# Kernel optimization log

Measured on AMD Instinct MI355X. Metric: run time of the kernel, lower is better.

The kernel has to match this reference:

```python
import jax, jax.numpy as jnp
import numpy as np

V, D, H, KV, L, FF, HD = 32000, 768, 12, 4, 4, 2048, 64
N_REP = H // KV  # 3
EPS = 1e-6
ROPE_THETA = 10000.0


def setup_inputs() -> dict:
    key = jax.random.key(0)
    ks = jax.random.split(key, 12)
    s = 0.02
    return {
        'idx': jax.random.randint(ks[0], (1, 2048), 0, V),
        'embed': jax.random.normal(ks[1], (V, D), jnp.float32) * s,
        'ln1_w': jnp.ones((L, D), jnp.float32),
        'Wq': jax.random.normal(ks[2], (L, D, H * HD), jnp.float32) * s,
        'Wk': jax.random.normal(ks[3], (L, D, KV * HD), jnp.float32) * s,
        'Wv': jax.random.normal(ks[4], (L, D, KV * HD), jnp.float32) * s,
        'Wo': jax.random.normal(ks[5], (L, H * HD, D), jnp.float32) * s,
        'ln2_w': jnp.ones((L, D), jnp.float32),
        'Wg': jax.random.normal(ks[6], (L, D, FF), jnp.float32) * s,
        'Wu': jax.random.normal(ks[7], (L, D, FF), jnp.float32) * s,
        'Wd': jax.random.normal(ks[8], (L, FF, D), jnp.float32) * s,
        'normf_w': jnp.ones((D,), jnp.float32),
    }


def _rms(x, w):
    xf = x.astype(jnp.float32)
    var = jnp.mean(xf * xf, axis=-1, keepdims=True)
    return w * (xf * jax.lax.rsqrt(var + EPS)).astype(x.dtype)


def _rotate_half(x):
    x1, x2 = x[..., : x.shape[-1] // 2], x[..., x.shape[-1] // 2:]
    return jnp.concatenate((-x2, x1), axis=-1)


def reference(idx, embed, ln1_w, Wq, Wk, Wv, Wo, ln2_w, Wg, Wu, Wd, normf_w):
    B, T = idx.shape
    x = embed[idx]  # [B,T,D]

    # RoPE tables: cos/sin [1,1,T,HD]
    inv_freq = 1.0 / (ROPE_THETA ** (jnp.arange(0, HD, 2, dtype=jnp.float32) / HD))
    pos = jnp.arange(T, dtype=jnp.float32)
    freqs = pos[:, None] * inv_freq[None, :]          # [T,HD/2]
    emb = jnp.concatenate((freqs, freqs), axis=-1)     # [T,HD]
    cos = jnp.cos(emb)[None, None].astype(x.dtype)
    sin = jnp.sin(emb)[None, None].astype(x.dtype)

    causal = jnp.tril(jnp.ones((T, T), bool))[None, None]  # [1,1,T,T]
    scale = 1.0 / np.sqrt(HD)

    for l in range(L):
        # --- attention ---
        h = _rms(x, ln1_w[l])
        q = (h @ Wq[l]).reshape(B, T, H, HD).transpose(0, 2, 1, 3)   # [B,H,T,HD]
        k = (h @ Wk[l]).reshape(B, T, KV, HD).transpose(0, 2, 1, 3)  # [B,KV,T,HD]
        v = (h @ Wv[l]).reshape(B, T, KV, HD).transpose(0, 2, 1, 3)
        q = q * cos + _rotate_half(q) * sin
        k = k * cos + _rotate_half(k) * sin
        k = jnp.repeat(k, N_REP, axis=1)  # [B,H,T,HD]
        v = jnp.repeat(v, N_REP, axis=1)
        scores = jnp.einsum('bhqd,bhkd->bhqk', q, k) * scale
        scores = jnp.where(causal, scores, -jnp.inf)
        probs = jax.nn.softmax(scores.astype(jnp.float32), axis=-1).astype(q.dtype)
        attn = jnp.einsum('bhqk,bhkd->bhqd', probs, v)
        attn = attn.transpose(0, 2, 1, 3).reshape(B, T, H * HD)
        x = x + attn @ Wo[l]
        # --- gated MLP ---
        h = _rms(x, ln2_w[l])
        x = x + (jax.nn.gelu(h @ Wg[l], approximate=True) * (h @ Wu[l])) @ Wd[l]

    x = _rms(x, normf_w)
    logits = (x @ embed.T).astype(jnp.float32)  # tied lm_head
    return logits
```

## Files before the change

### kernel.cpp

```cpp
#include <hip/hip_runtime.h>

#define TSEQ 2048
#define DM   768
#define NH   12
#define NKV  4
#define HD   64
#define FFD  2048
#define NL   4
#define VOC  32000
#define QKVN 1280

typedef __attribute__((ext_vector_type(8))) short short8;
typedef __attribute__((ext_vector_type(4))) float f32x4;

__device__ __forceinline__ unsigned short f2b(float f) {
  unsigned int u = __float_as_uint(f);
  u += 0x7fffu + ((u >> 16) & 1u);
  return (unsigned short)(u >> 16);
}
__device__ __forceinline__ float b2f(unsigned short u) {
  return __uint_as_float(((unsigned int)u) << 16);
}
__device__ __forceinline__ unsigned int packbf(float a, float b) {
  return (unsigned int)f2b(a) | ((unsigned int)f2b(b) << 16);
}

__device__ __forceinline__ void gl16(const unsigned short* g, unsigned short* l) {
  __builtin_amdgcn_global_load_lds(
      (const __attribute__((address_space(1))) void*)g,
      (__attribute__((address_space(3))) void*)l, 16, 0, 0);
}

__global__ void cast_bf16_kernel(const float* __restrict__ src,
                                 unsigned short* __restrict__ dst, int n4) {
  int i = blockIdx.x * blockDim.x + threadIdx.x;
  if (i >= n4) return;
  float4 v = ((const float4*)src)[i];
  uint2 o; o.x = packbf(v.x, v.y); o.y = packbf(v.z, v.w);
  ((uint2*)dst)[i] = o;
}

__global__ void rope_tab_kernel(float2* __restrict__ tab) {
  int i = blockIdx.x * blockDim.x + threadIdx.x;
  int pos = i >> 5, d = i & 31;
  float inv = exp2f(-(float)d * (13.287712379549449f / 32.0f));
  float sv, cv; sincosf((float)pos * inv, &sv, &cv);
  tab[i] = make_float2(cv, sv);
}

__global__ void transpose_all_kernel(const float* __restrict__ Wq, const float* __restrict__ Wk,
                                     const float* __restrict__ Wv, const float* __restrict__ Wo,
                                     const float* __restrict__ Wg, const float* __restrict__ Wu,
                                     const float* __restrict__ Wd, unsigned short* __restrict__ wts,
                                     size_t LW) {
  __shared__ float tile[32][33];
  int r = blockIdx.x, l = blockIdx.z;
  const float* src; size_t sstr, doff; int K, N, nx;
  if (r < 576)       { src = Wq; sstr = 589824;  doff = 0;                          K = 768;  N = 768;  nx = 24; }
  else if (r < 768)  { src = Wk; sstr = 196608;  doff = 768ull * 768;               K = 768;  N = 256;  nx = 8;  r -= 576; }
  else if (r < 960)  { src = Wv; sstr = 196608;  doff = 1024ull * 768;              K = 768;  N = 256;  nx = 8;  r -= 768; }
  else if (r < 1536) { src = Wo; sstr = 589824;  doff = (size_t)QKVN * DM;          K = 768;  N = 768;  nx = 24; r -= 960; }
  else if (r < 3072) { src = Wg; sstr = 1572864; doff = (size_t)QKVN * DM + (size_t)DM * DM;
                       K = 768;  N = 2048; nx = 64; r -= 1536; }
  else if (r < 4608) { src = Wu; sstr = 1572864; doff = (size_t)QKVN * DM + (size_t)DM * DM + (size_t)FFD * DM;
                       K = 768;  N = 2048; nx = 64; r -= 3072; }
  else               { src = Wd; sstr = 1572864; doff = (size_t)QKVN * DM + (size_t)DM * DM + 2ull * FFD * DM;
                       K = 2048; N = 768;  nx = 24; r -= 4608; }
  int bx = r % nx, by = r / nx;
  src += (size_t)l * sstr;
  unsigned short* dst = wts + (size_t)l * LW + doff;
  int n0 = bx * 32, k0 = by * 32;
  int tx = threadIdx.x, ty = threadIdx.y;
  #pragma unroll
  for (int i = 0; i < 4; ++i) {
    int rr = ty + i * 8;
    tile[rr][tx] = src[(size_t)(k0 + rr) * N + n0 + tx];
  }
  __syncthreads();
  #pragma unroll
  for (int i = 0; i < 4; ++i) {
    int rr = ty + i * 8;
    dst[(size_t)(n0 + rr) * K + k0 + tx] = f2b(tile[tx][rr]);
  }
}

__global__ void gather_kernel(const int* __restrict__ idx,
                              const float* __restrict__ embed,
                              float* __restrict__ x) {
  int row = blockIdx.x; int t = threadIdx.x;
  int id = idx[row];
  ((float4*)(x + (size_t)row * DM))[t] = ((const float4*)(embed + (size_t)id * DM))[t];
}

__global__ void rmsnorm_kernel(const float* __restrict__ x,
                               const float* __restrict__ w,
                               unsigned short* __restrict__ out) {
  int row = blockIdx.x; int t = threadIdx.x;
  const float* xr = x + (size_t)row * DM;
  float v0 = xr[t], v1 = xr[t + 256], v2 = xr[t + 512];
  float s = v0*v0 + v1*v1 + v2*v2;
  #pragma unroll
  for (int off = 1; off < 64; off <<= 1) s += __shfl_xor(s, off);
  __shared__ float red[4];
  if ((t & 63) == 0) red[t >> 6] = s;
  __syncthreads();
  float tot = red[0] + red[1] + red[2] + red[3];
  float rs = rsqrtf(tot * (1.0f / DM) + 1e-6f);
  unsigned short* orow = out + (size_t)row * DM;
  orow[t]       = f2b(w[t]       * v0 * rs);
  orow[t + 256] = f2b(w[t + 256] * v1 * rs);
  orow[t + 512] = f2b(w[t + 512] * v2 * rs);
}

__global__ __launch_bounds__(512, 1) void gemm_l8_kernel(
    const unsigned short* __restrict__ A, const unsigned short* __restrict__ Bt,
    float* __restrict__ C, int N, int K) {
  __shared__ unsigned short lds[2][2][256 * 64];
  const int NT = K >> 6;
  int bid = blockIdx.x, nwg = gridDim.x;
  int wgid = (bid & 7) * (nwg >> 3) + (bid >> 3);
  int m0 = (wgid & 7) * 256;
  int n0 = (wgid >> 3) * 256;
  int tid = threadIdx.x;
  int lane = tid & 63, w = tid >> 6;
  int wm = w >> 2, wn = w & 3;
  int al = lane & 15, ag = lane >> 4;
  int swz = (al & 7) << 3;

  int rA = tid >> 3;
  int cK = ((tid & 7) * 8) ^ ((rA & 7) << 3);
  const unsigned short* Ag = A + (size_t)(m0 + rA) * K + cK;
  const unsigned short* Bg = Bt + (size_t)(n0 + rA) * K + cK;

  f32x4 acc[8][4];
  #pragma unroll
  for (int i = 0; i < 8; ++i)
    #pragma unroll
    for (int n = 0; n < 4; ++n) acc[i][n] = (f32x4){0.f, 0.f, 0.f, 0.f};

  #define STAGE(kt, c) { \
    size_t ko = (size_t)(kt) * 64; \
    unsigned short* dA = &lds[(c)][0][0] + w * 512; \
    unsigned short* dB = &lds[(c)][1][0] + w * 512; \
    gl16(Ag + (size_t)0   * K + ko, dA);            \
    gl16(Ag + (size_t)64  * K + ko, dA + 4096);     \
    gl16(Ag + (size_t)128 * K + ko, dA + 8192);     \
    gl16(Ag + (size_t)192 * K + ko, dA + 12288);    \
    gl16(Bg + (size_t)0   * K + ko, dB);            \
    gl16(Bg + (size_t)64  * K + ko, dB + 4096);     \
    gl16(Bg + (size_t)128 * K + ko, dB + 8192);     \
    gl16(Bg + (size_t)192 * K + ko, dB + 12288);    \
  }

  STAGE(0, 0);
  STAGE(1, 1);
  asm volatile("s_waitcnt vmcnt(8)" ::: "memory");
  __builtin_amdgcn_s_barrier();

  for (int t = 0; t < NT; ++t) {
    int cur = t & 1;
    const unsigned short* La = &lds[cur][0][0];
    const unsigned short* Lb = &lds[cur][1][0];
    short8 a0[8], b0[4], a1[8], b1[4];
    #pragma unroll
    for (int i = 0; i < 4; ++i)
      a0[i] = *(const short8*)&La[(wm*128 + i*16 + al)*64 + ((ag*8) ^ swz)];
    #pragma unroll
    for (int n = 0; n < 4; ++n)
      b0[n] = *(const short8*)&Lb[(wn*64 + n*16 + al)*64 + ((ag*8) ^ swz)];
    #pragma unroll
    for (int i = 4; i < 8; ++i)
      a0[i] = *(const short8*)&La[(wm*128 + i*16 + al)*64 + ((ag*8) ^ swz)];
    asm volatile("s_waitcnt lgkmcnt(4)" ::: "memory");
    __builtin_amdgcn_sched_barrier(0);
    #pragma unroll
    for (int i = 0; i < 4; ++i)
      #pragma unroll
      for (int n = 0; n < 4; ++n)
        acc[i][n] = __builtin_amdgcn_mfma_f32_16x16x32_bf16(a0[i], b0[n], acc[i][n], 0, 0, 0);
    #pragma unroll
    for (int n = 0; n < 4; ++n)
      b1[n] = *(const short8*)&Lb[(wn*64 + n*16 + al)*64 + ((32 + ag*8) ^ swz)];
    #pragma unroll
    for (int i = 0; i < 4; ++i)
      a1[i] = *(const short8*)&La[(wm*128 + i*16 + al)*64 + ((32 + ag*8) ^ swz)];
    asm volatile("s_waitcnt lgkmcnt(8)" ::: "memory");
    __builtin_amdgcn_sched_barrier(0);
    #pragma unroll
    for (int i = 4; i < 8; ++i)
      #pragma unroll
      for (int n = 0; n < 4; ++n)
        acc[i][n] = __builtin_amdgcn_mfma_f32_16x16x32_bf16(a0[i], b0[n], acc[i][n], 0, 0, 0);
    #pragma unroll
    for (int i = 4; i < 8; ++i)
      a1[i] = *(const short8*)&La[(wm*128 + i*16 + al)*64 + ((32 + ag*8) ^ swz)];
    asm volatile("s_waitcnt lgkmcnt(4)" ::: "memory");
    __builtin_amdgcn_sched_barrier(0);
    #pragma unroll
    for (int i = 0; i < 4; ++i)
      #pragma unroll
      for (int n = 0; n < 4; ++n)
        acc[i][n] = __builtin_amdgcn_mfma_f32_16x16x32_bf16(a1[i], b1[n], acc[i][n], 0, 0, 0);
    asm volatile("s_waitcnt lgkmcnt(0)" ::: "memory");
    __builtin_amdgcn_sched_barrier(0);
    __builtin_amdgcn_s_barrier();
    if (t + 2 < NT) STAGE(t + 2, cur);
    __builtin_amdgcn_s_setprio(1);
    #pragma unroll
    for (int i = 4; i < 8; ++i)
      #pragma unroll
      for (int n = 0; n < 4; ++n)
        acc[i][n] = __builtin_amdgcn_mfma_f32_16x16x32_bf16(a1[i], b1[n], acc[i][n], 0, 0, 0);
    __builtin_amdgcn_s_setprio(0);
    if (t + 2 < NT) { asm volatile("s_waitcnt vmcnt(8)" ::: "memory"); }
    else            { asm volatile("s_waitcnt vmcnt(0)" ::: "memory"); }
    __builtin_amdgcn_s_barrier();
  }
  #undef STAGE

  #pragma unroll
  for (int i = 0; i < 8; ++i)
    #pragma unroll
    for (int r = 0; r < 4; ++r) {
      float* Cr = C + (size_t)(m0 + wm*128 + i*16 + ag*4 + r) * N + n0 + wn*64 + al;
      #pragma unroll
      for (int n = 0; n < 4; ++n) Cr[n * 16] = acc[i][n][r];
    }
}

__global__ __launch_bounds__(512) void gemm_p8_kernel(
    const unsigned short* __restrict__ A, const unsigned short* __restrict__ Bt,
    float* __restrict__ C, int N, int K, int Kc) {
  __shared__ unsigned short lds[2][2][128 * 64];
  const int NT = Kc >> 6;
  int bid = blockIdx.x, nwg = gridDim.x;
  int wgid = (bid & 7) * (nwg >> 3) + (bid >> 3);
  int m0 = (wgid & 15) * 128;
  int n0 = (wgid >> 4) * 128;
  int tid = threadIdx.x;
  int lane = tid & 63, w = tid >> 6;
  int wm = w >> 2, wn = w & 3;
  int al = lane & 15, ag = lane >> 4;
  int swz = (al & 7) << 3;

  size_t koff = (size_t)blockIdx.y * Kc;
  int rp = 8 * w + (lane >> 3);
  int cK = ((lane & 7) * 8) ^ ((lane >> 3) << 3);
  const unsigned short* Ag = A + (size_t)(m0 + rp) * K + koff + cK;
  const unsigned short* Bg = Bt + (size_t)(n0 + rp) * K + koff + cK;

  f32x4 acc[4][2];
  #pragma unroll
  for (int i = 0; i < 4; ++i)
    #pragma unroll
    for (int n = 0; n < 2; ++n) acc[i][n] = (f32x4){0.f, 0.f, 0.f, 0.f};

  #define STAGE(kt, c) { \
    size_t ko = (size_t)(kt) * 64; \
    unsigned short* dA = &lds[(c)][0][0] + w * 512; \
    unsigned short* dB = &lds[(c)][1][0] + w * 512; \
    gl16(Ag + ko,                 dA);        \
    gl16(Ag + (size_t)64*K + ko,  dA + 4096); \
    gl16(Bg + ko,                 dB);        \
    gl16(Bg + (size_t)64*K + ko,  dB + 4096); \
  }

  STAGE(0, 0);
  STAGE(1, 1);
  asm volatile("s_waitcnt vmcnt(4)" ::: "memory");
  __builtin_amdgcn_s_barrier();

  for (int t = 0; t < NT; ++t) {
    int cur = t & 1;
    const unsigned short* La = &lds[cur][0][0];
    const unsigned short* Lb = &lds[cur][1][0];
    short8 a0[4], b0[2], a1[4], b1[2];
    #pragma unroll
    for (int i = 0; i < 4; ++i)
      a0[i] = *(const short8*)&La[(wm*64 + i*16 + al)*64 + ((ag*8) ^ swz)];
    #pragma unroll
    for (int n = 0; n < 2; ++n)
      b0[n] = *(const short8*)&Lb[(wn*32 + n*16 + al)*64 + ((ag*8) ^ swz)];
    #pragma unroll
    for (int i = 0; i < 4; ++i)
      a1[i] = *(const short8*)&La[(wm*64 + i*16 + al)*64 + ((32 + ag*8) ^ swz)];
    #pragma unroll
    for (int n = 0; n < 2; ++n)
      b1[n] = *(const short8*)&Lb[(wn*32 + n*16 + al)*64 + ((32 + ag*8) ^ swz)];
    asm volatile("s_waitcnt lgkmcnt(6)" ::: "memory");
    __builtin_amdgcn_sched_barrier(0);
    #pragma unroll
    for (int i = 0; i < 4; ++i)
      #pragma unroll
      for (int n = 0; n < 2; ++n)
        acc[i][n] = __builtin_amdgcn_mfma_f32_16x16x32_bf16(a0[i], b0[n], acc[i][n], 0, 0, 0);
    asm volatile("s_waitcnt lgkmcnt(0)" ::: "memory");
    __builtin_amdgcn_sched_barrier(0);
    __builtin_amdgcn_s_barrier();
    if (t + 2 < NT) STAGE(t + 2, cur);
    __builtin_amdgcn_s_setprio(1);
    #pragma unroll
    for (int i = 0; i < 4; ++i)
      #pragma unroll
      for (int n = 0; n < 2; ++n)
        acc[i][n] = __builtin_amdgcn_mfma_f32_16x16x32_bf16(a1[i], b1[n], acc[i][n], 0, 0, 0);
    __builtin_amdgcn_s_setprio(0);
    if (t + 2 < NT) { asm volatile("s_waitcnt vmcnt(4)" ::: "memory"); }
    else            { asm volatile("s_waitcnt vmcnt(0)" ::: "memory"); }
    __builtin_amdgcn_s_barrier();
  }
  #undef STAGE

  #pragma unroll
  for (int i = 0; i < 4; ++i)
    #pragma unroll
    for (int r = 0; r < 4; ++r) {
      float* Cr = C + (size_t)(m0 + wm*64 + i*16 + ag*4 + r) * N + n0 + wn*32 + al;
      #pragma unroll
      for (int n = 0; n < 2; ++n) atomicAdd(&Cr[n * 16], acc[i][n][r]);
    }
}

__device__ __forceinline__ float gelu_t(float x) {
  float x3 = x * x * x;
  return 0.5f * x * (1.0f + tanhf(0.7978845608028654f * (x + 0.044715f * x3)));
}

__global__ __launch_bounds__(512) void gemm_gu8_kernel(
    const unsigned short* __restrict__ A, const unsigned short* __restrict__ BtG,
    const unsigned short* __restrict__ BtU, unsigned short* __restrict__ Cm) {
  __shared__ unsigned short lds[2][3][128 * 64];
  const int K = DM;
  const int NT = K >> 6;
  int bid = blockIdx.x, nwg = gridDim.x;
  int wgid = (bid & 7) * (nwg >> 3) + (bid >> 3);
  int m0 = (wgid & 15) * 128;
  int n0 = (wgid >> 4) * 128;
  int tid = threadIdx.x;
  int lane = tid & 63, w = tid >> 6;
  int wm = w >> 2, wn = w & 3;
  int al = lane & 15, ag = lane >> 4;
  int swz = (al & 7) << 3;

  int rp = 8 * w + (lane >> 3);
  int cK = ((lane & 7) * 8) ^ ((lane >> 3) << 3);
  const unsigned short* Ag = A + (size_t)(m0 + rp) * K + cK;
  const unsigned short* Gg = BtG + (size_t)(n0 + rp) * K + cK;
  const unsigned short* Ug = BtU + (size_t)(n0 + rp) * K + cK;

  f32x4 accg[4][2], accu[4][2];
  #pragma unroll
  for (int i = 0; i < 4; ++i)
    #pragma unroll
    for (int n = 0; n < 2; ++n) {
      accg[i][n] = (f32x4){0.f, 0.f, 0.f, 0.f};
      accu[i][n] = (f32x4){0.f, 0.f, 0.f, 0.f};
    }

  #define STAGE(kt, c) { \
    size_t ko = (size_t)(kt) * 64; \
    unsigned short* dA = &lds[(c)][0][0] + w * 512; \
    unsigned short* dG = &lds[(c)][1][0] + w * 512; \
    unsigned short* dU = &lds[(c)][2][0] + w * 512; \
    gl16(Ag + ko,                 dA);        \
    gl16(Ag + (size_t)64*K + ko,  dA + 4096); \
    gl16(Gg + ko,                 dG);        \
    gl16(Gg + (size_t)64*K + ko,  dG + 4096); \
    gl16(Ug + ko,                 dU);        \
    gl16(Ug + (size_t)64*K + ko,  dU + 4096); \
  }

  STAGE(0, 0);
  STAGE(1, 1);
  asm volatile("s_waitcnt vmcnt(6)" ::: "memory");
  __builtin_amdgcn_s_barrier();

  for (int t = 0; t < NT; ++t) {
    int cur = t & 1;
    const unsigned short* La = &lds[cur][0][0];
    const unsigned short* Lg = &lds[cur][1][0];
    const unsigned short* Lu = &lds[cur][2][0];
    short8 a0[4], g0[2], u0[2], a1[4], g1[2], u1[2];
    #pragma unroll
    for (int i = 0; i < 4; ++i)
      a0[i] = *(const short8*)&La[(wm*64 + i*16 + al)*64 + ((ag*8) ^ swz)];
    #pragma unroll
    for (int n = 0; n < 2; ++n) {
      g0[n] = *(const short8*)&Lg[(wn*32 + n*16 + al)*64 + ((ag*8) ^ swz)];
      u0[n] = *(const short8*)&Lu[(wn*32 + n*16 + al)*64 + ((ag*8) ^ swz)];
    }
    #pragma unroll
    for (int i = 0; i < 4; ++i)
      a1[i] = *(const short8*)&La[(wm*64 + i*16 + al)*64 + ((32 + ag*8) ^ swz)];
    #pragma unroll
    for (int n = 0; n < 2; ++n) {
      g1[n] = *(const short8*)&Lg[(wn*32 + n*16 + al)*64 + ((32 + ag*8) ^ swz)];
      u1[n] = *(const short8*)&Lu[(wn*32 + n*16 + al)*64 + ((32 + ag*8) ^ swz)];
    }
    asm volatile("s_waitcnt lgkmcnt(8)" ::: "memory");
    __builtin_amdgcn_sched_barrier(0);
    #pragma unroll
    for (int i = 0; i < 4; ++i)
      #pragma unroll
      for (int n = 0; n < 2; ++n) {
        accg[i][n] = __builtin_amdgcn_mfma_f32_16x16x32_bf16(a0[i], g0[n], accg[i][n], 0, 0, 0);
        accu[i][n] = __builtin_amdgcn_mfma_f32_16x16x32_bf16(a0[i], u0[n], accu[i][n], 0, 0, 0);
      }
    asm volatile("s_waitcnt lgkmcnt(0)" ::: "memory");
    __builtin_amdgcn_sched_barrier(0);
    __builtin_amdgcn_s_barrier();
    if (t + 2 < NT) STAGE(t + 2, cur);
    __builtin_amdgcn_s_setprio(1);
    #pragma unroll
    for (int i = 0; i < 4; ++i)
      #pragma unroll
      for (int n = 0; n < 2; ++n) {
        accg[i][n] = __builtin_amdgcn_mfma_f32_16x16x32_bf16(a1[i], g1[n], accg[i][n], 0, 0, 0);
        accu[i][n] = __builtin_amdgcn_mfma_f32_16x16x32_bf16(a1[i], u1[n], accu[i][n], 0, 0, 0);
      }
    __builtin_amdgcn_s_setprio(0);
    if (t + 2 < NT) { asm volatile("s_waitcnt vmcnt(6)" ::: "memory"); }
    else            { asm volatile("s_waitcnt vmcnt(0)" ::: "memory"); }
    __builtin_amdgcn_s_barrier();
  }
  #undef STAGE

  #pragma unroll
  for (int i = 0; i < 4; ++i)
    #pragma unroll
    for (int r = 0; r < 4; ++r) {
      unsigned short* Cr = Cm + (size_t)(m0 + wm*64 + i*16 + ag*4 + r) * FFD + n0 + wn*32 + al;
      #pragma unroll
      for (int n = 0; n < 2; ++n)
        Cr[n * 16] = f2b(gelu_t(accg[i][n][r]) * accu[i][n][r]);
    }
}

__global__ __launch_bounds__(256) void gemm_qkv_kernel(
    const unsigned short* __restrict__ A, const unsigned short* __restrict__ Bt,
    unsigned short* __restrict__ C, unsigned short* __restrict__ vT,
    const float2* __restrict__ rope_tab) {
  const int N = QKVN, K = DM;
  __shared__ unsigned short As[128 * 40];
  __shared__ unsigned short Bs[128 * 40];
  int bid = blockIdx.x, nwg = gridDim.x;
  int wgid = (bid & 7) * (nwg >> 3) + (bid >> 3);
  int m0 = (wgid & 15) * 128;
  int n0 = (wgid >> 4) * 128;
  int tid = threadIdx.x;
  int lane = tid & 63, wave = tid >> 6;
  int wr = (wave >> 1) * 64, wc = (wave & 1) * 64;
  int l16 = lane & 15, lk8 = (lane >> 4) * 8;
  f32x4 acc[4][4];
  #pragma unroll
  for (int m = 0; m < 4; ++m)
    #pragma unroll
    for (int n = 0; n < 4; ++n) acc[m][n] = (f32x4){0.f, 0.f, 0.f, 0.f};
  const unsigned short* Abase = A + (size_t)m0 * K;
  const unsigned short* Bbase = Bt + (size_t)n0 * K;
  int r0 = tid >> 2;
  int c0 = (tid & 3) * 8;
  for (int k0 = 0; k0 < K; k0 += 32) {
    uint4 a0 = *(const uint4*)(Abase + (size_t)r0 * K + k0 + c0);
    uint4 a1 = *(const uint4*)(Abase + (size_t)(r0 + 64) * K + k0 + c0);
    uint4 b0 = *(const uint4*)(Bbase + (size_t)r0 * K + k0 + c0);
    uint4 b1 = *(const uint4*)(Bbase + (size_t)(r0 + 64) * K + k0 + c0);
    *(uint4*)&As[r0 * 40 + c0] = a0;
    *(uint4*)&As[(r0 + 64) * 40 + c0] = a1;
    *(uint4*)&Bs[r0 * 40 + c0] = b0;
    *(uint4*)&Bs[(r0 + 64) * 40 + c0] = b1;
    __syncthreads();
    short8 af[4], bfr[4];
    #pragma unroll
    for (int m = 0; m < 4; ++m) af[m]  = *(const short8*)&As[(wr + m*16 + l16) * 40 + lk8];
    #pragma unroll
    for (int n = 0; n < 4; ++n) bfr[n] = *(const short8*)&Bs[(wc + n*16 + l16) * 40 + lk8];
    #pragma unroll
    for (int m = 0; m < 4; ++m)
      #pragma unroll
      for (int n = 0; n < 4; ++n)
        acc[m][n] = __builtin_amdgcn_mfma_f32_16x16x32_bf16(af[m], bfr[n], acc[m][n], 0, 0, 0);
    __syncthreads();
  }
  bool qk = (n0 + wc) < 1024;
  #pragma unroll
  for (int m = 0; m < 4; ++m)
    #pragma unroll
    for (int r = 0; r < 4; ++r) {
      int pos = m0 + wr + m*16 + ((lane >> 4) << 2) + r;
      if (qk) {
        unsigned short* Cr = C + (size_t)pos * N + n0 + wc + l16;
        #pragma unroll
        for (int n = 0; n < 2; ++n) {
          int d = n * 16 + l16;
          float2 cs = rope_tab[pos * 32 + d];
          float x1 = acc[m][n][r], x2 = acc[m][n + 2][r];
          Cr[n * 16]       = f2b(x1 * cs.x - x2 * cs.y);
          Cr[(n + 2) * 16] = f2b(x2 * cs.x + x1 * cs.y);
        }
      } else {
        #pragma unroll
        for (int n = 0; n < 4; ++n) {
          int hb = n0 + wc + n*16 + l16 - 1024;
          vT[(size_t)hb * TSEQ + pos] = f2b(acc[m][n][r]);
        }
      }
    }
}

__global__ __launch_bounds__(256) void attn_chunk_kernel(
    const unsigned short* __restrict__ qkv, const unsigned short* __restrict__ vT,
    unsigned short* __restrict__ out, float* __restrict__ pO, float* __restrict__ pML) {
  __shared__ unsigned short Ks[2][64 * 64];
  __shared__ unsigned short Vt[2][64 * 64];
  __shared__ unsigned short Ps[4][16 * 64];
  int s = blockIdx.x, h = blockIdx.y;
  int qt, ci;
  if (s < 8)       { qt = s;                ci = 0; }
  else if (s < 24) { qt = 8 + ((s-8) >> 1); ci = (s-8) & 1; }
  else if (s < 48) { qt = 16 + (s-24) / 3;  ci = (s-24) % 3; }
  else             { qt = 24 + ((s-48) >> 2); ci = (s-48) & 3; }
  int nt = qt + 1;
  int t0 = ci * 8;
  int t1 = t0 + 8; if (t1 > nt) t1 = nt;
  int cnt = (nt + 7) >> 3;
  int r0 = qt * 64;
  int kvh = h / 3;
  int t = threadIdx.x;
  int lane = t & 63, w = t >> 6;
  int l16 = lane & 15, g = lane >> 4;

  int qr = r0 + w * 16 + l16;
  const unsigned short* qrow = qkv + (size_t)qr * QKVN + h * HD;
  short8 aq0 = *(const short8*)(qrow + 8 * g);
  short8 aq1 = *(const short8*)(qrow + 32 + 8 * g);

  int sw = (lane & 7) ^ (lane >> 3);
  int rloc = w * 16 + (lane >> 3);
  const unsigned short* kgb = qkv + (size_t)rloc * QKVN + DM + kvh * HD + 8 * sw;
  const unsigned short* vgb = vT + (size_t)(kvh * 64 + rloc) * TSEQ + 8 * sw;

  #define ASTAGE(kb, c) { \
    unsigned short* kd = &Ks[(c)][0] + w * 1024; \
    unsigned short* vd = &Vt[(c)][0] + w * 1024; \
    gl16(kgb + (size_t)(kb) * QKVN,       kd);       \
    gl16(kgb + (size_t)((kb) + 8) * QKVN, kd + 512); \
    gl16(vgb + (kb),                      vd);       \
    gl16(vgb + (size_t)8 * TSEQ + (kb),   vd + 512); \
  }

  f32x4 o_acc[4];
  float mrun[4], lsum[4];
  #pragma unroll
  for (int i = 0; i < 4; ++i) { o_acc[i] = (f32x4){0.f,0.f,0.f,0.f}; mrun[i] = -1e30f; lsum[i] = 0.f; }

  ASTAGE(t0 * 64, 0);
  for (int kt = t0; kt < t1; ++kt) {
    int cur = (kt - t0) & 1;
    int kb = kt * 64;
    if (kt + 1 < t1) {
      ASTAGE((kt + 1) * 64, cur ^ 1);
      asm volatile("s_waitcnt vmcnt(4)" ::: "memory");
    } else {
      asm volatile("s_waitcnt vmcnt(0)" ::: "memory");
    }
    __builtin_amdgcn_s_barrier();

    const unsigned short* Kc = &Ks[cur][0];
    const unsigned short* Vc = &Vt[cur][0];

    f32x4 s_acc[4];
    #pragma unroll
    for (int nb = 0; nb < 4; ++nb) s_acc[nb] = (f32x4){0.f,0.f,0.f,0.f};
    #pragma unroll
    for (int nb = 0; nb < 4; ++nb) {
      int key = nb * 16 + l16;
      short8 bk0 = *(const short8*)&Kc[key * 64 + ((g       ^ (key & 7)) << 3)];
      short8 bk1 = *(const short8*)&Kc[key * 64 + (((4 + g) ^ (key & 7)) << 3)];
      s_acc[nb] = __builtin_amdgcn_mfma_f32_16x16x32_bf16(aq0, bk0, s_acc[nb], 0, 0, 0);
      s_acc[nb] = __builtin_amdgcn_mfma_f32_16x16x32_bf16(aq1, bk1, s_acc[nb], 0, 0, 0);
    }

    bool diag = (kt == qt);
    #pragma unroll
    for (int r = 0; r < 4; ++r) {
      int qg = r0 + w * 16 + g * 4 + r;
      float sv[4];
      #pragma unroll
      for (int nb = 0; nb < 4; ++nb) {
        sv[nb] = s_acc[nb][r] * 0.125f;
        if (diag && (kb + nb * 16 + l16 > qg)) sv[nb] = -1e30f;
      }
      float mx = fmaxf(fmaxf(sv[0], sv[1]), fmaxf(sv[2], sv[3]));
      mx = fmaxf(mx, __shfl_xor(mx, 1));
      mx = fmaxf(mx, __shfl_xor(mx, 2));
      mx = fmaxf(mx, __shfl_xor(mx, 4));
      mx = fmaxf(mx, __shfl_xor(mx, 8));
      if (mx > mrun[r] + 8.0f) {
        float es = __expf(mrun[r] - mx);
        lsum[r] *= es;
        #pragma unroll
        for (int db = 0; db < 4; ++db) o_acc[db][r] *= es;
        mrun[r] = mx;
      }
      float rsum = 0.f;
      #pragma unroll
      for (int nb = 0; nb < 4; ++nb) { sv[nb] = __expf(sv[nb] - mrun[r]); rsum += sv[nb]; }
      lsum[r] += rsum;
      int qloc = g * 4 + r, q7 = qloc & 7;
      #pragma unroll
      for (int nb = 0; nb < 4; ++nb) {
        int key = nb * 16 + l16;
        Ps[w][qloc * 64 + ((((key >> 3) ^ q7) << 3) + (key & 7))] = f2b(sv[nb]);
      }
    }

    #pragma unroll
    for (int kc = 0; kc < 2; ++kc) {
      short8 pa = *(const short8*)&Ps[w][l16 * 64 + (((4 * kc + g) ^ (l16 & 7)) << 3)];
      #pragma unroll
      for (int db = 0; db < 4; ++db) {
        int d = db * 16 + l16;
        short8 bv = *(const short8*)&Vc[d * 64 + (((4 * kc + g) ^ (d & 7)) << 3)];
        o_acc[db] = __builtin_amdgcn_mfma_f32_16x16x32_bf16(pa, bv, o_acc[db], 0, 0, 0);
      }
    }
    __builtin_amdgcn_s_barrier();
  }
  #undef ASTAGE

  if (cnt == 1) {
    #pragma unroll
    for (int r = 0; r < 4; ++r) {
      int qg = r0 + w * 16 + g * 4 + r;
      float sr = lsum[r];
      sr += __shfl_xor(sr, 1);
      sr += __shfl_xor(sr, 2);
      sr += __shfl_xor(sr, 4);
      sr += __shfl_xor(sr, 8);
      float inv = 1.0f / sr;
      unsigned short* orow = out + (size_t)qg * DM + h * HD + l16;
      #pragma unroll
      for (int db = 0; db < 4; ++db) orow[db * 16] = f2b(o_acc[db][r] * inv);
    }
  } else {
    size_t slotg = (size_t)h * 80 + s;
    float* po = pO + slotg * 4096;
    float* pm = pML + slotg * 128;
    #pragma unroll
    for (int r = 0; r < 4; ++r) {
      int row = w * 16 + g * 4 + r;
      float sr = lsum[r];
      sr += __shfl_xor(sr, 1);
      sr += __shfl_xor(sr, 2);
      sr += __shfl_xor(sr, 4);
      sr += __shfl_xor(sr, 8);
      #pragma unroll
      for (int db = 0; db < 4; ++db) po[row * 64 + db * 16 + l16] = o_acc[db][r];
      if (l16 == 0) { pm[row * 2] = mrun[r]; pm[row * 2 + 1] = sr; }
    }
  }
}

__global__ __launch_bounds__(256) void attn_combine_kernel(
    const float* __restrict__ pO, const float* __restrict__ pML,
    unsigned short* __restrict__ out) {
  int h = blockIdx.y;
  int qt = 8 + blockIdx.x;
  int base, cnt;
  if (qt < 16)      { base = 8 + (qt - 8) * 2;  cnt = 2; }
  else if (qt < 24) { base = 24 + (qt - 16) * 3; cnt = 3; }
  else              { base = 48 + (qt - 24) * 4; cnt = 4; }
  int t = threadIdx.x;
  int row = t >> 2, d0 = (t & 3) * 16;
  float m[4], l[4];
  float M = -1e30f;
  for (int c = 0; c < cnt; ++c) {
    const float* pm = pML + ((size_t)h * 80 + base + c) * 128 + row * 2;
    m[c] = pm[0]; l[c] = pm[1];
    M = fmaxf(M, m[c]);
  }
  float o[16];
  #pragma unroll
  for (int j = 0; j < 16; ++j) o[j] = 0.f;
  float wl = 0.f;
  for (int c = 0; c < cnt; ++c) {
    float wc = __expf(m[c] - M);
    wl += wc * l[c];
    const float4* po = (const float4*)(pO + ((size_t)h * 80 + base + c) * 4096 + row * 64 + d0);
    #pragma unroll
    for (int q = 0; q < 4; ++q) {
      float4 v = po[q];
      o[q*4+0] += wc * v.x; o[q*4+1] += wc * v.y;
      o[q*4+2] += wc * v.z; o[q*4+3] += wc * v.w;
    }
  }
  float inv = 1.0f / wl;
  unsigned short* orow = out + (size_t)(qt * 64 + row) * DM + h * HD + d0;
  uint4 s0, s1;
  s0.x = packbf(o[0]*inv,  o[1]*inv);  s0.y = packbf(o[2]*inv,  o[3]*inv);
  s0.z = packbf(o[4]*inv,  o[5]*inv);  s0.w = packbf(o[6]*inv,  o[7]*inv);
  s1.x = packbf(o[8]*inv,  o[9]*inv);  s1.y = packbf(o[10]*inv, o[11]*inv);
  s1.z = packbf(o[12]*inv, o[13]*inv); s1.w = packbf(o[14]*inv, o[15]*inv);
  ((uint4*)orow)[0] = s0; ((uint4*)orow)[1] = s1;
}

extern "C" void kernel_launch(void* const* d_in, const int* in_sizes, int n_in,
                              void* d_out, int out_size, void* d_ws, size_t ws_size,
                              hipStream_t stream) {
  const int*   idx   = (const int*)d_in[0];
  const float* embed = (const float*)d_in[1];
  const float* ln1   = (const float*)d_in[2];
  const float* Wq    = (const float*)d_in[3];
  const float* Wk    = (const float*)d_in[4];
  const float* Wv    = (const float*)d_in[5];
  const float* Wo    = (const float*)d_in[6];
  const float* ln2   = (const float*)d_in[7];
  const float* Wg    = (const float*)d_in[8];
  const float* Wu    = (const float*)d_in[9];
  const float* Wd    = (const float*)d_in[10];
  const float* normf = (const float*)d_in[11];
  float* out = (float*)d_out;
  char* ws = (char*)d_ws;
  (void)in_sizes; (void)n_in; (void)out_size; (void)ws_size;

  unsigned short* embed_bf = (unsigned short*)ws;
  size_t off = (size_t)VOC * DM * 2;
  unsigned short* wts = (unsigned short*)(ws + off);
  const size_t LW = (size_t)QKVN * DM + (size_t)DM * DM
                  + 2ull * FFD * DM + (size_t)DM * FFD;
  off += LW * 2ull * NL;
  float* xf = (float*)(ws + off);            off += (size_t)TSEQ * DM * 4;
  unsigned short* h_bf = (unsigned short*)(ws + off);    off += (size_t)TSEQ * DM * 2;
  unsigned short* qkv_bf = (unsigned short*)(ws + off);  off += (size_t)TSEQ * QKVN * 2;
  unsigned short* attn_bf = (unsigned short*)(ws + off); off += (size_t)TSEQ * DM * 2;
  float* pO = (float*)(ws + off);
  unsigned short* m_bf = (unsigned short*)(ws + off);
  off += (size_t)NH * 80 * 4096 * 4;
  float* pML = (float*)(ws + off);           off += (size_t)NH * 80 * 128 * 4;
  float2* rope_tab = (float2*)(ws + off);    off += (size_t)TSEQ * 32 * 8;
  unsigned short* vT = (unsigned short*)(ws + off);      off += (size_t)NKV * HD * TSEQ * 2;

  cast_bf16_kernel<<<(VOC * DM / 4 + 255) / 256, 256, 0, stream>>>(embed, embed_bf, VOC * DM / 4);
  rope_tab_kernel<<<TSEQ * 32 / 256, 256, 0, stream>>>(rope_tab);
  transpose_all_kernel<<<dim3(6144, 1, NL), dim3(32, 8), 0, stream>>>(
      Wq, Wk, Wv, Wo, Wg, Wu, Wd, wts, LW);

  gather_kernel<<<TSEQ, 192, 0, stream>>>(idx, embed, xf);

  for (int l = 0; l < NL; ++l) {
    unsigned short* base = wts + (size_t)l * LW;
    unsigned short* qkvT = base;
    unsigned short* woT  = base + (size_t)QKVN * DM;
    unsigned short* wguT = woT + (size_t)DM * DM;
    unsigned short* wdT  = wguT + 2ull * FFD * DM;

    rmsnorm_kernel<<<TSEQ, 256, 0, stream>>>(xf, ln1 + (size_t)l * DM, h_bf);
    gemm_qkv_kernel<<<(QKVN / 128) * 16, 256, 0, stream>>>(h_bf, qkvT, qkv_bf, vT, rope_tab);
    attn_chunk_kernel<<<dim3(80, NH), 256, 0, stream>>>(qkv_bf, vT, attn_bf, pO, pML);
    attn_combine_kernel<<<dim3(24, NH), 256, 0, stream>>>(pO, pML, attn_bf);
    gemm_p8_kernel<<<dim3((DM / 128) * 16, 3), 512, 0, stream>>>(attn_bf, woT, xf, DM, DM, 256);
    rmsnorm_kernel<<<TSEQ, 256, 0, stream>>>(xf, ln2 + (size_t)l * DM, h_bf);
    gemm_gu8_kernel<<<(FFD / 128) * 16, 512, 0, stream>>>(h_bf, wguT, wguT + (size_t)FFD * DM, m_bf);
    gemm_p8_kernel<<<dim3((DM / 128) * 16, 4), 512, 0, stream>>>(m_bf, wdT, xf, DM, FFD, 512);
  }

  rmsnorm_kernel<<<TSEQ, 256, 0, stream>>>(xf, normf, h_bf);
  gemm_l8_kernel<<<(VOC / 256) * (TSEQ / 256), 512, 0, stream>>>(h_bf, embed_bf, out, VOC, DM);
}
```

Baseline: 760.6 us.

## Pipeline QKV GEMM with async LDS loads and merge prep kernels into one

Replaces the simple synchronous QKV GEMM with a 512-thread, 8-wave kernel. It double-buffers swizzled LDS tiles through global_load_lds and interleaves MFMA with the prefetch. The V-transpose epilogue now goes through LDS scratch so it writes coalesced 16-byte stores instead of scattered 2-byte ones. The four setup kernels (embed cast, rope table, weight transpose, gather) are fused into one launch to cut launch overhead. The cost is more code complexity and a large single prep grid with divergent block roles.

New measurement: 695.9 us. -8.5%, faster.

```diff
diff --git a/kernel.cpp b/kernel.cpp
--- a/kernel.cpp
+++ b/kernel.cpp
@@ -31,30 +31,42 @@
       (__attribute__((address_space(3))) void*)l, 16, 0, 0);
 }
 
-__global__ void cast_bf16_kernel(const float* __restrict__ src,
-                                 unsigned short* __restrict__ dst, int n4) {
-  int i = blockIdx.x * blockDim.x + threadIdx.x;
-  if (i >= n4) return;
-  float4 v = ((const float4*)src)[i];
-  uint2 o; o.x = packbf(v.x, v.y); o.y = packbf(v.z, v.w);
-  ((uint2*)dst)[i] = o;
-}
-
-__global__ void rope_tab_kernel(float2* __restrict__ tab) {
-  int i = blockIdx.x * blockDim.x + threadIdx.x;
-  int pos = i >> 5, d = i & 31;
-  float inv = exp2f(-(float)d * (13.287712379549449f / 32.0f));
-  float sv, cv; sincosf((float)pos * inv, &sv, &cv);
-  tab[i] = make_float2(cv, sv);
-}
-
-__global__ void transpose_all_kernel(const float* __restrict__ Wq, const float* __restrict__ Wk,
-                                     const float* __restrict__ Wv, const float* __restrict__ Wo,
-                                     const float* __restrict__ Wg, const float* __restrict__ Wu,
-                                     const float* __restrict__ Wd, unsigned short* __restrict__ wts,
-                                     size_t LW) {
+__global__ void mega_prep_kernel(const float* __restrict__ embed, unsigned short* __restrict__ embed_bf,
+                                 float2* __restrict__ rope_tab,
+                                 const int* __restrict__ idx, float* __restrict__ xf,
+                                 const float* __restrict__ Wq, const float* __restrict__ Wk,
+                                 const float* __restrict__ Wv, const float* __restrict__ Wo,
+                                 const float* __restrict__ Wg, const float* __restrict__ Wu,
+                                 const float* __restrict__ Wd, unsigned short* __restrict__ wts,
+                                 size_t LW) {
+  int blk = blockIdx.x;
+  int t = threadIdx.x;
+  if (blk < 24000) {
+    int i = blk * 256 + t;
+    float4 v = ((const float4*)embed)[i];
+    uint2 o; o.x = packbf(v.x, v.y); o.y = packbf(v.z, v.w);
+    ((uint2*)embed_bf)[i] = o;
+    return;
+  }
+  if (blk < 24256) {
+    int i = (blk - 24000) * 256 + t;
+    int pos = i >> 5, d = i & 31;
+    float inv = exp2f(-(float)d * (13.287712379549449f / 32.0f));
+    float sv, cv; sincosf((float)pos * inv, &sv, &cv);
+    rope_tab[i] = make_float2(cv, sv);
+    return;
+  }
+  if (blk < 26304) {
+    int row = blk - 24256;
+    if (t < 192) {
+      int id = idx[row];
+      ((float4*)(xf + (size_t)row * DM))[t] = ((const float4*)(embed + (size_t)id * DM))[t];
+    }
+    return;
+  }
   __shared__ float tile[32][33];
-  int r = blockIdx.x, l = blockIdx.z;
+  int r = blk - 26304;
+  int l = r / 6144; r -= l * 6144;
   const float* src; size_t sstr, doff; int K, N, nx;
   if (r < 576)       { src = Wq; sstr = 589824;  doff = 0;                          K = 768;  N = 768;  nx = 24; }
   else if (r < 768)  { src = Wk; sstr = 196608;  doff = 768ull * 768;               K = 768;  N = 256;  nx = 8;  r -= 576; }
@@ -70,7 +82,7 @@
   src += (size_t)l * sstr;
   unsigned short* dst = wts + (size_t)l * LW + doff;
   int n0 = bx * 32, k0 = by * 32;
-  int tx = threadIdx.x, ty = threadIdx.y;
+  int tx = t & 31, ty = t >> 5;
   #pragma unroll
   for (int i = 0; i < 4; ++i) {
     int rr = ty + i * 8;
@@ -82,14 +94,6 @@
     int rr = ty + i * 8;
     dst[(size_t)(n0 + rr) * K + k0 + tx] = f2b(tile[tx][rr]);
   }
-}
-
-__global__ void gather_kernel(const int* __restrict__ idx,
-                              const float* __restrict__ embed,
-                              float* __restrict__ x) {
-  int row = blockIdx.x; int t = threadIdx.x;
-  int id = idx[row];
-  ((float4*)(x + (size_t)row * DM))[t] = ((const float4*)(embed + (size_t)id * DM))[t];
 }
 
 __global__ void rmsnorm_kernel(const float* __restrict__ x,
@@ -436,76 +440,129 @@
     }
 }
 
-__global__ __launch_bounds__(256) void gemm_qkv_kernel(
+__global__ __launch_bounds__(512) void gemm_qkv8_kernel(
     const unsigned short* __restrict__ A, const unsigned short* __restrict__ Bt,
     unsigned short* __restrict__ C, unsigned short* __restrict__ vT,
     const float2* __restrict__ rope_tab) {
+  __shared__ unsigned short lds[2][2][128 * 64];
   const int N = QKVN, K = DM;
-  __shared__ unsigned short As[128 * 40];
-  __shared__ unsigned short Bs[128 * 40];
+  const int NT = K >> 6;
   int bid = blockIdx.x, nwg = gridDim.x;
   int wgid = (bid & 7) * (nwg >> 3) + (bid >> 3);
   int m0 = (wgid & 15) * 128;
   int n0 = (wgid >> 4) * 128;
   int tid = threadIdx.x;
-  int lane = tid & 63, wave = tid >> 6;
-  int wr = (wave >> 1) * 64, wc = (wave & 1) * 64;
-  int l16 = lane & 15, lk8 = (lane >> 4) * 8;
-  f32x4 acc[4][4];
-  #pragma unroll
-  for (int m = 0; m < 4; ++m)
-    #pragma unroll
-    for (int n = 0; n < 4; ++n) acc[m][n] = (f32x4){0.f, 0.f, 0.f, 0.f};
-  const unsigned short* Abase = A + (size_t)m0 * K;
-  const unsigned short* Bbase = Bt + (size_t)n0 * K;
-  int r0 = tid >> 2;
-  int c0 = (tid & 3) * 8;
-  for (int k0 = 0; k0 < K; k0 += 32) {
-    uint4 a0 = *(const uint4*)(Abase + (size_t)r0 * K + k0 + c0);
-    uint4 a1 = *(const uint4*)(Abase + (size_t)(r0 + 64) * K + k0 + c0);
-    uint4 b0 = *(const uint4*)(Bbase + (size_t)r0 * K + k0 + c0);
-    uint4 b1 = *(const uint4*)(Bbase + (size_t)(r0 + 64) * K + k0 + c0);
-    *(uint4*)&As[r0 * 40 + c0] = a0;
-    *(uint4*)&As[(r0 + 64) * 40 + c0] = a1;
-    *(uint4*)&Bs[r0 * 40 + c0] = b0;
-    *(uint4*)&Bs[(r0 + 64) * 40 + c0] = b1;
-    __syncthreads();
-    short8 af[4], bfr[4];
-    #pragma unroll
-    for (int m = 0; m < 4; ++m) af[m]  = *(const short8*)&As[(wr + m*16 + l16) * 40 + lk8];
-    #pragma unroll
-    for (int n = 0; n < 4; ++n) bfr[n] = *(const short8*)&Bs[(wc + n*16 + l16) * 40 + lk8];
-    #pragma unroll
-    for (int m = 0; m < 4; ++m)
+  int lane = tid & 63, w = tid >> 6;
+  int wm = w >> 1, wn = w & 1;
+  int al = lane & 15, ag = lane >> 4;
+  int swz = (al & 7) << 3;
+
+  int rp = 8 * w + (lane >> 3);
+  int cK = ((lane & 7) * 8) ^ ((lane >> 3) << 3);
+  const unsigned short* Ag = A + (size_t)(m0 + rp) * K + cK;
+  const unsigned short* Bg = Bt + (size_t)(n0 + rp) * K + cK;
+
+  f32x4 acc[2][4];
+  #pragma unroll
+  for (int i = 0; i < 2; ++i)
+    #pragma unroll
+    for (int n = 0; n < 4; ++n) acc[i][n] = (f32x4){0.f, 0.f, 0.f, 0.f};
+
+  #define STAGE(kt, c) { \
+    size_t ko = (size_t)(kt) * 64; \
+    unsigned short* dA = &lds[(c)][0][0] + w * 512; \
+    unsigned short* dB = &lds[(c)][1][0] + w * 512; \
+    gl16(Ag + ko,                 dA);        \
+    gl16(Ag + (size_t)64*K + ko,  dA + 4096); \
+    gl16(Bg + ko,                 dB);        \
+    gl16(Bg + (size_t)64*K + ko,  dB + 4096); \
+  }
+
+  STAGE(0, 0);
+  STAGE(1, 1);
+  asm volatile("s_waitcnt vmcnt(4)" ::: "memory");
+  __builtin_amdgcn_s_barrier();
+
+  for (int t = 0; t < NT; ++t) {
+    int cur = t & 1;
+    const unsigned short* La = &lds[cur][0][0];
+    const unsigned short* Lb = &lds[cur][1][0];
+    short8 a0[2], b0[4], a1[2], b1[4];
+    #pragma unroll
+    for (int i = 0; i < 2; ++i)
+      a0[i] = *(const short8*)&La[(wm*32 + i*16 + al)*64 + ((ag*8) ^ swz)];
+    #pragma unroll
+    for (int n = 0; n < 4; ++n)
+      b0[n] = *(const short8*)&Lb[(wn*64 + n*16 + al)*64 + ((ag*8) ^ swz)];
+    #pragma unroll
+    for (int i = 0; i < 2; ++i)
+      a1[i] = *(const short8*)&La[(wm*32 + i*16 + al)*64 + ((32 + ag*8) ^ swz)];
+    #pragma unroll
+    for (int n = 0; n < 4; ++n)
+      b1[n] = *(const short8*)&Lb[(wn*64 + n*16 + al)*64 + ((32 + ag*8) ^ swz)];
+    asm volatile("s_waitcnt lgkmcnt(6)" ::: "memory");
+    __builtin_amdgcn_sched_barrier(0);
+    #pragma unroll
+    for (int i = 0; i < 2; ++i)
       #pragma unroll
       for (int n = 0; n < 4; ++n)
-        acc[m][n] = __builtin_amdgcn_mfma_f32_16x16x32_bf16(af[m], bfr[n], acc[m][n], 0, 0, 0);
-    __syncthreads();
-  }
-  bool qk = (n0 + wc) < 1024;
-  #pragma unroll
-  for (int m = 0; m < 4; ++m)
-    #pragma unroll
-    for (int r = 0; r < 4; ++r) {
-      int pos = m0 + wr + m*16 + ((lane >> 4) << 2) + r;
-      if (qk) {
-        unsigned short* Cr = C + (size_t)pos * N + n0 + wc + l16;
+        acc[i][n] = __builtin_amdgcn_mfma_f32_16x16x32_bf16(a0[i], b0[n], acc[i][n], 0, 0, 0);
+    asm volatile("s_waitcnt lgkmcnt(0)" ::: "memory");
+    __builtin_amdgcn_sched_barrier(0);
+    __builtin_amdgcn_s_barrier();
+    if (t + 2 < NT) STAGE(t + 2, cur);
+    __builtin_amdgcn_s_setprio(1);
+    #pragma unroll
+    for (int i = 0; i < 2; ++i)
+      #pragma unroll
+      for (int n = 0; n < 4; ++n)
+        acc[i][n] = __builtin_amdgcn_mfma_f32_16x16x32_bf16(a1[i], b1[n], acc[i][n], 0, 0, 0);
+    __builtin_amdgcn_s_setprio(0);
+    if (t + 2 < NT) { asm volatile("s_waitcnt vmcnt(4)" ::: "memory"); }
+    else            { asm volatile("s_waitcnt vmcnt(0)" ::: "memory"); }
+    __builtin_amdgcn_s_barrier();
+  }
+  #undef STAGE
+
+  bool qk = (n0 + wn * 64) < 1024;
+  if (qk) {
+    #pragma unroll
+    for (int i = 0; i < 2; ++i)
+      #pragma unroll
+      for (int r = 0; r < 4; ++r) {
+        int pos = m0 + wm*32 + i*16 + ag*4 + r;
+        unsigned short* Cr = C + (size_t)pos * N + n0 + wn*64 + al;
         #pragma unroll
         for (int n = 0; n < 2; ++n) {
-          int d = n * 16 + l16;
+          int d = n * 16 + al;
           float2 cs = rope_tab[pos * 32 + d];
-          float x1 = acc[m][n][r], x2 = acc[m][n + 2][r];
+          float x1 = acc[i][n][r], x2 = acc[i][n + 2][r];
           Cr[n * 16]       = f2b(x1 * cs.x - x2 * cs.y);
           Cr[(n + 2) * 16] = f2b(x2 * cs.x + x1 * cs.y);
         }
-      } else {
+      }
+  } else {
+    unsigned short* scr = &lds[0][0][0] + w * 2048;
+    #pragma unroll
+    for (int i = 0; i < 2; ++i)
+      #pragma unroll
+      for (int r = 0; r < 4; ++r) {
+        int posl = i*16 + ag*4 + r;
         #pragma unroll
-        for (int n = 0; n < 4; ++n) {
-          int hb = n0 + wc + n*16 + l16 - 1024;
-          vT[(size_t)hb * TSEQ + pos] = f2b(acc[m][n][r]);
-        }
+        for (int n = 0; n < 4; ++n)
+          scr[(n*16 + al) * 32 + posl] = f2b(acc[i][n][r]);
       }
-    }
+    asm volatile("s_waitcnt lgkmcnt(0)" ::: "memory");
+    int hb0 = n0 + wn * 64 - 1024;
+    int pos0 = m0 + wm * 32;
+    #pragma unroll
+    for (int j = 0; j < 4; ++j) {
+      int col = (lane >> 2) + j * 16;
+      int pc  = (lane & 3) * 8;
+      uint4 v = *(const uint4*)&scr[col * 32 + pc];
+      *(uint4*)&vT[(size_t)(hb0 + col) * TSEQ + pos0 + pc] = v;
+    }
+  }
 }
 
 __global__ __launch_bounds__(256) void attn_chunk_kernel(
@@ -741,12 +798,8 @@
   float2* rope_tab = (float2*)(ws + off);    off += (size_t)TSEQ * 32 * 8;
   unsigned short* vT = (unsigned short*)(ws + off);      off += (size_t)NKV * HD * TSEQ * 2;
 
-  cast_bf16_kernel<<<(VOC * DM / 4 + 255) / 256, 256, 0, stream>>>(embed, embed_bf, VOC * DM / 4);
-  rope_tab_kernel<<<TSEQ * 32 / 256, 256, 0, stream>>>(rope_tab);
-  transpose_all_kernel<<<dim3(6144, 1, NL), dim3(32, 8), 0, stream>>>(
-      Wq, Wk, Wv, Wo, Wg, Wu, Wd, wts, LW);
-
-  gather_kernel<<<TSEQ, 192, 0, stream>>>(idx, embed, xf);
+  mega_prep_kernel<<<26304 + 6144 * NL, 256, 0, stream>>>(
+      embed, embed_bf, rope_tab, idx, xf, Wq, Wk, Wv, Wo, Wg, Wu, Wd, wts, LW);
 
   for (int l = 0; l < NL; ++l) {
     unsigned short* base = wts + (size_t)l * LW;
@@ -756,7 +809,7 @@
     unsigned short* wdT  = wguT + 2ull * FFD * DM;
 
     rmsnorm_kernel<<<TSEQ, 256, 0, stream>>>(xf, ln1 + (size_t)l * DM, h_bf);
-    gemm_qkv_kernel<<<(QKVN / 128) * 16, 256, 0, stream>>>(h_bf, qkvT, qkv_bf, vT, rope_tab);
+    gemm_qkv8_kernel<<<(QKVN / 128) * 16, 512, 0, stream>>>(h_bf, qkvT, qkv_bf, vT, rope_tab);
     attn_chunk_kernel<<<dim3(80, NH), 256, 0, stream>>>(qkv_bf, vT, attn_bf, pO, pML);
     attn_combine_kernel<<<dim3(24, NH), 256, 0, stream>>>(pO, pML, attn_bf);
     gemm_p8_kernel<<<dim3((DM / 128) * 16, 3), 512, 0, stream>>>(attn_bf, woT, xf, DM, DM, 256);
```
